# Kernel optimization log

Measured on AMD Instinct MI355X. Metric: run time of the kernel, lower is better.

Reference implementation:

```python
import jax, jax.numpy as jnp
import numpy as np

N_HEAD = 8
HEAD_DIM = 64
DIM = 512
INNER = N_HEAD * HEAD_DIM
ATT_THRESHOLD = 1e-4
SCALE = HEAD_DIM ** -0.5


def setup_inputs() -> dict:
    key = jax.random.key(0)
    ks = jax.random.split(key, 7)
    b, n, dn = 2, 2048, 2048
    fr = jax.random.normal(ks[0], (b, n, DIM), dtype=jnp.float32)
    dt = jax.random.normal(ks[1], (b, dn, DIM), dtype=jnp.float32)
    s = DIM ** -0.5
    Wq = jax.random.normal(ks[2], (DIM, INNER), dtype=jnp.float32) * s
    Wk = jax.random.normal(ks[3], (DIM, INNER), dtype=jnp.float32) * s
    Wv = jax.random.normal(ks[4], (DIM, INNER), dtype=jnp.float32) * s
    Wo = jax.random.normal(ks[5], (INNER, DIM), dtype=jnp.float32) * (INNER ** -0.5)
    bo = jax.random.normal(ks[6], (DIM,), dtype=jnp.float32) * 0.01
    return {"fr": fr, "dt": dt, "Wq": Wq, "Wk": Wk, "Wv": Wv, "Wo": Wo, "bo": bo}


def reference(fr, dt, Wq, Wk, Wv, Wo, bo):
    b, n, _ = fr.shape
    dn = dt.shape[1]
    # projections -> [b, seq, n_head, head_dim]
    q = (fr @ Wq).reshape(b, n, N_HEAD, HEAD_DIM)
    k = (dt @ Wk).reshape(b, dn, N_HEAD, HEAD_DIM)
    v = (dt @ Wv).reshape(b, dn, N_HEAD, HEAD_DIM)
    # full attention matrix [b, h, n, dn]
    scores = jnp.einsum('bihd,bjhd->bhij', q, k) * SCALE
    attn = jax.nn.softmax(scores, axis=-1)
    # torch .clip(t) with one positional arg clamps the MIN: max(attn, t)
    attn = jnp.maximum(attn, ATT_THRESHOLD) - ATT_THRESHOLD
    attn = attn / jnp.sum(attn, axis=-1, keepdims=True)
    out = jnp.einsum('bhij,bjhd->bihd', attn, v).reshape(b, n, INNER)
    return out @ Wo + bo
```

## Files before the change

### kernel.cpp

```cpp
#include <hip/hip_runtime.h>
#include <hip/hip_bf16.h>

#define BB 2
#define SEQ 2048
#define NHEAD 8
#define HD 64
#define ATT_T 1e-4f
#define QSCALE 0.18033688011112042f

typedef short s16x8 __attribute__((ext_vector_type(8)));
typedef float f32x16 __attribute__((ext_vector_type(16)));

#define MFMA32(a, b, c) __builtin_amdgcn_mfma_f32_32x32x16_bf16((a), (b), (c), 0, 0, 0)
#define EXP2(x) __builtin_amdgcn_exp2f(x)

__device__ __forceinline__ unsigned short bfr(float x) {
  __hip_bfloat16 h = __float2bfloat16(x);
  return __builtin_bit_cast(unsigned short, h);
}
__device__ __forceinline__ unsigned int packbf(float a, float b) {
  return (unsigned int)bfr(a) | ((unsigned int)bfr(b) << 16);
}
__device__ __forceinline__ void async16(const void* g, void* l) {
  __builtin_amdgcn_global_load_lds(
      (const __attribute__((address_space(1))) unsigned int*)g,
      (__attribute__((address_space(3))) unsigned int*)l, 16, 0, 0);
}

__global__ __launch_bounds__(256) void convT(const float* __restrict__ w0,
                                             const float* __restrict__ w1,
                                             const float* __restrict__ w2,
                                             const float* __restrict__ w3,
                                             unsigned short* __restrict__ o0,
                                             unsigned short* __restrict__ o1,
                                             unsigned short* __restrict__ o2,
                                             unsigned short* __restrict__ o3) {
  __shared__ float tle[64][65];
  const float* W = blockIdx.z == 0 ? w0 : blockIdx.z == 1 ? w1 : blockIdx.z == 2 ? w2 : w3;
  unsigned short* WT = blockIdx.z == 0 ? o0 : blockIdx.z == 1 ? o1 : blockIdx.z == 2 ? o2 : o3;
  const int r0 = blockIdx.y * 64, c0 = blockIdx.x * 64;
  const int tr = threadIdx.x >> 4;
  const int tc = threadIdx.x & 15;
  #pragma unroll
  for (int i = 0; i < 4; i++) {
    int r = tr + i * 16;
    float4 v = *(const float4*)(W + (size_t)(r0 + r) * 512 + c0 + tc * 4);
    tle[r][tc * 4 + 0] = v.x;
    tle[r][tc * 4 + 1] = v.y;
    tle[r][tc * 4 + 2] = v.z;
    tle[r][tc * 4 + 3] = v.w;
  }
  __syncthreads();
  #pragma unroll
  for (int i = 0; i < 4; i++) {
    int c = tr + i * 16;
    int rr = tc * 4;
    uint2 p;
    p.x = packbf(tle[rr + 0][c], tle[rr + 1][c]);
    p.y = packbf(tle[rr + 2][c], tle[rr + 3][c]);
    *(uint2*)(WT + (size_t)(c0 + c) * 512 + r0 + rr) = p;
  }
}

__global__ __launch_bounds__(256) void gemm_qkv(const float* __restrict__ frF,
                                                const float* __restrict__ dtF,
                                                const unsigned short* __restrict__ WqT,
                                                const unsigned short* __restrict__ WkT,
                                                const unsigned short* __restrict__ WvT,
                                                unsigned short* __restrict__ Qp,
                                                unsigned short* __restrict__ Kp,
                                                unsigned short* __restrict__ VTp) {
  __shared__ __align__(16) unsigned short smem[12288];
  unsigned short* Asm = smem;
  unsigned short* Bsm = smem + 4096;

  const int tid = threadIdx.x, lane = tid & 63, w = tid >> 6;
  const int l31 = lane & 31, lh = lane >> 5;
  const int m0 = blockIdx.y * 64, n0 = blockIdx.x * 128;
  const int z = blockIdx.z;
  const float* A = z == 0 ? frF : dtF;
  const unsigned short* BT = z == 0 ? WqT : (z == 1 ? WkT : WvT);
  unsigned short* OP = z == 0 ? Qp : (z == 1 ? Kp : VTp);
  const float scale = z == 0 ? QSCALE : 1.0f;

  const int arow = tid >> 2, arun = tid & 3;
  const float* Ap = A + (size_t)(m0 + arow) * 512 + arun * 8;
  const int aoff = (arow >> 5) * 1024 + (arun >> 1) * 512 + (arun & 1) * 256 + (arow & 31) * 8;

  auto stageB = [&](int kt, int buf) {
    const int k0 = kt * 32;
    #pragma unroll
    for (int i = 0; i < 2; i++) {
      int id = w * 2 + i;
      int g2 = id >> 1, ks = id & 1;
      async16(BT + (size_t)(n0 + g2 * 32 + l31) * 512 + k0 + ks * 16 + lh * 8,
              Bsm + buf * 4096 + g2 * 1024 + ks * 512);
    }
  };

  f32x16 acc[2];
  #pragma unroll
  for (int j = 0; j < 2; j++)
    #pragma unroll
    for (int r = 0; r < 16; r++) acc[j][r] = 0.f;

  float4 a0 = *(const float4*)(Ap + 0);
  float4 a1 = *(const float4*)(Ap + 4);
  stageB(0, 0);
  {
    uint4 w4;
    w4.x = packbf(a0.x, a0.y); w4.y = packbf(a0.z, a0.w);
    w4.z = packbf(a1.x, a1.y); w4.w = packbf(a1.z, a1.w);
    *(uint4*)(Asm + aoff) = w4;
  }
  a0 = *(const float4*)(Ap + 32);
  a1 = *(const float4*)(Ap + 36);

  for (int kt = 0; kt < 16; ++kt) {
    __syncthreads();
    if (kt + 1 < 16) {
      const int nb = (kt + 1) & 1;
      stageB(kt + 1, nb);
      uint4 w4;
      w4.x = packbf(a0.x, a0.y); w4.y = packbf(a0.z, a0.w);
      w4.z = packbf(a1.x, a1.y); w4.w = packbf(a1.z, a1.w);
      *(uint4*)(Asm + nb * 2048 + aoff) = w4;
      if (kt + 2 < 16) {
        a0 = *(const float4*)(Ap + (kt + 2) * 32);
        a1 = *(const float4*)(Ap + (kt + 2) * 32 + 4);
      }
    }
    const int buf = kt & 1;
    #pragma unroll
    for (int ks = 0; ks < 2; ++ks) {
      s16x8 af = *(const s16x8*)(Asm + buf * 2048 + (w & 1) * 1024 + ks * 512 + lane * 8);
      s16x8 b0 = *(const s16x8*)(Bsm + buf * 4096 + ((w >> 1) * 2 + 0) * 1024 + ks * 512 + lane * 8);
      s16x8 b1 = *(const s16x8*)(Bsm + buf * 4096 + ((w >> 1) * 2 + 1) * 1024 + ks * 512 + lane * 8);
      acc[0] = MFMA32(af, b0, acc[0]);
      acc[1] = MFMA32(af, b1, acc[1]);
    }
  }

  const int wm = (w & 1) * 32, wn = (w >> 1) * 64;
  const int bb = m0 >> 11, s0 = m0 & 2047;
  __syncthreads();
  if (z <= 1) {
    #pragma unroll
    for (int j = 0; j < 2; j++)
      #pragma unroll
      for (int r = 0; r < 16; r++) {
        int mm = wm + (r & 3) + 8 * (r >> 2) + 4 * lh;
        int nn = wn + j * 32 + l31;
        smem[mm * 136 + nn] = bfr(acc[j][r] * scale);
      }
    __syncthreads();
    #pragma unroll
    for (int it = 0; it < 4; ++it) {
      int c = tid + it * 256;
      int mm = c >> 4, seg = c & 15;
      uint4 vdat = *(const uint4*)(smem + mm * 136 + seg * 8);
      int n = n0 + seg * 8, h = n >> 6, d = n & 63;
      *(uint4*)(OP + ((size_t)((bb * NHEAD + h) * SEQ + s0 + mm)) * HD + d) = vdat;
    }
  } else {
    #pragma unroll
    for (int j = 0; j < 2; j++)
      #pragma unroll
      for (int r = 0; r < 16; r += 2) {
        int mm = wm + (r & 3) + 8 * (r >> 2) + 4 * lh;
        int nn = wn + j * 32 + l31;
        *(unsigned int*)(smem + nn * 72 + mm) = packbf(acc[j][r], acc[j][r + 1]);
      }
    __syncthreads();
    #pragma unroll
    for (int it = 0; it < 4; ++it) {
      int c = tid + it * 256;
      int nn = c >> 3, seg = c & 7;
      uint4 vdat = *(const uint4*)(smem + nn * 72 + seg * 8);
      int n = n0 + nn, h = n >> 6, d = n & 63;
      *(uint4*)(OP + ((size_t)((bb * NHEAD + h) * HD + d)) * SEQ + s0 + seg * 8) = vdat;
    }
  }
}

__device__ __forceinline__ void gemm_core64x128(const unsigned short* __restrict__ A,
                                                const unsigned short* __restrict__ BT,
                                                unsigned short* smem, int m0, int n0,
                                                int w, int lane, f32x16 (&acc)[2]) {
  unsigned short* Asm = smem;
  unsigned short* Bsm = smem + 4096;
  const int l31 = lane & 31, lh = lane >> 5;

  auto stage = [&](int kt, int buf) {
    const int k0 = kt * 32;
    #pragma unroll
    for (int i = 0; i < 3; i++) {
      int id = w * 3 + i;
      if (id < 4) {
        int g = id >> 1, ks = id & 1;
        async16(A + (size_t)(m0 + g * 32 + l31) * 512 + k0 + ks * 16 + lh * 8,
                Asm + buf * 2048 + g * 1024 + ks * 512);
      } else {
        int id2 = id - 4, g = id2 >> 1, ks = id2 & 1;
        async16(BT + (size_t)(n0 + g * 32 + l31) * 512 + k0 + ks * 16 + lh * 8,
                Bsm + buf * 4096 + g * 1024 + ks * 512);
      }
    }
  };

  stage(0, 0);
  for (int kt = 0; kt < 16; ++kt) {
    __syncthreads();
    if (kt + 1 < 16) stage(kt + 1, (kt + 1) & 1);
    const int buf = kt & 1;
    #pragma unroll
    for (int ks = 0; ks < 2; ++ks) {
      s16x8 af = *(const s16x8*)(Asm + buf * 2048 + (w & 1) * 1024 + ks * 512 + lane * 8);
      s16x8 b0 = *(const s16x8*)(Bsm + buf * 4096 + ((w >> 1) * 2 + 0) * 1024 + ks * 512 + lane * 8);
      s16x8 b1 = *(const s16x8*)(Bsm + buf * 4096 + ((w >> 1) * 2 + 1) * 1024 + ks * 512 + lane * 8);
      acc[0] = MFMA32(af, b0, acc[0]);
      acc[1] = MFMA32(af, b1, acc[1]);
    }
  }
}

__global__ __launch_bounds__(256) void gemm_out(const unsigned short* __restrict__ A,
                                                const unsigned short* __restrict__ BT,
                                                const float* __restrict__ bias,
                                                float* __restrict__ O) {
  __shared__ __align__(16) unsigned short smem[12288];
  const int tid = threadIdx.x, lane = tid & 63, w = tid >> 6;
  const int l31 = lane & 31, lh = lane >> 5;
  const int m0 = blockIdx.y * 64, n0 = blockIdx.x * 128;

  f32x16 acc[2];
  #pragma unroll
  for (int j = 0; j < 2; j++)
    #pragma unroll
    for (int r = 0; r < 16; r++) acc[j][r] = 0.f;

  gemm_core64x128(A, BT, smem, m0, n0, w, lane, acc);

  const int wm = (w & 1) * 32, wn = (w >> 1) * 64;
  #pragma unroll
  for (int j = 0; j < 2; j++) {
    float bv = bias[n0 + wn + j * 32 + l31];
    #pragma unroll
    for (int r = 0; r < 16; r++) {
      int mm = wm + (r & 3) + 8 * (r >> 2) + 4 * lh;
      O[(size_t)(m0 + mm) * 512 + n0 + wn + j * 32 + l31] = acc[j][r] + bv;
    }
  }
}

__global__ __launch_bounds__(512, 4) void attn_mfma(const unsigned short* __restrict__ Q,
                                                    const unsigned short* __restrict__ K,
                                                    const unsigned short* __restrict__ VT,
                                                    unsigned short* __restrict__ O) {
  __shared__ __align__(16) unsigned short kls[4][2][2048];
  __shared__ __align__(16) unsigned short vls[4][2][2048];
  __shared__ float larr[4][2][32];
  __shared__ float warr[4][2][32];

  const int tid = threadIdx.x;
  const int lane = tid & 63;
  const int w = tid >> 6;
  const int wq = w & 1, wk = w >> 1;
  const int l31 = lane & 31, lh = lane >> 5;

  const int qt = blockIdx.x & 31;
  const int bh = blockIdx.x >> 5;

  const unsigned short* Qh = Q + (size_t)bh * SEQ * HD;
  const unsigned short* Kh = K + (size_t)bh * SEQ * HD;
  const unsigned short* VTh = VT + (size_t)bh * HD * SEQ;

  const int qrow = qt * 64 + wq * 32 + l31;
  s16x8 qf[4];
  #pragma unroll
  for (int t = 0; t < 4; t++)
    qf[t] = *(const s16x8*)(Qh + (size_t)qrow * HD + 16 * t + 8 * lh);

  const int kbase = wk * 512;

  float l = 0.f;
  #pragma unroll
  for (int i = 0; i < 2; i++) {
    int tt = wq * 2 + i;
    async16(Kh + (size_t)(kbase + l31) * HD + tt * 16 + lh * 8, &kls[wk][0][tt * 512]);
  }
  for (int c = 0; c < 16; ++c) {
    __syncthreads();
    const int buf = c & 1;
    if (c + 1 < 16) {
      int key0 = kbase + (c + 1) * 32;
      #pragma unroll
      for (int i = 0; i < 2; i++) {
        int tt = wq * 2 + i;
        async16(Kh + (size_t)(key0 + l31) * HD + tt * 16 + lh * 8,
                &kls[wk][buf ^ 1][tt * 512]);
      }
    }
    f32x16 sc;
    #pragma unroll
    for (int r = 0; r < 16; r++) sc[r] = 0.f;
    #pragma unroll
    for (int tt = 0; tt < 4; tt++) {
      s16x8 kf = *(const s16x8*)&kls[wk][buf][tt * 512 + lane * 8];
      sc = MFMA32(kf, qf[tt], sc);
    }
    float s0 = 0.f, s1 = 0.f, s2 = 0.f, s3 = 0.f;
    #pragma unroll
    for (int r = 0; r < 4; r++) {
      s0 += EXP2(sc[r]);
      s1 += EXP2(sc[4 + r]);
      s2 += EXP2(sc[8 + r]);
      s3 += EXP2(sc[12 + r]);
    }
    l += (s0 + s1) + (s2 + s3);
  }
  l += __shfl_xor(l, 32);
  if (lh == 0) larr[wk][wq][l31] = l;

  f32x16 acc[2];
  #pragma unroll
  for (int j = 0; j < 2; j++)
    #pragma unroll
    for (int r = 0; r < 16; r++) acc[j][r] = 0.f;
  float wacc = 0.f;
  float tl = 0.f;

  #pragma unroll
  for (int i = 0; i < 2; i++) {
    int tt = wq * 2 + i;
    async16(Kh + (size_t)(kbase + l31) * HD + tt * 16 + lh * 8, &kls[wk][0][tt * 512]);
    async16(VTh + (size_t)(wq * 32 + l31) * SEQ + kbase + i * 16 + lh * 8,
            &vls[wk][0][(wq * 2 + i) * 512]);
  }
  for (int c = 0; c < 16; ++c) {
    __syncthreads();
    if (c == 0) {
      tl = ATT_T * (larr[0][wq][l31] + larr[1][wq][l31] +
                    larr[2][wq][l31] + larr[3][wq][l31]);
    }
    const int buf = c & 1;
    if (c + 1 < 16) {
      int key0 = kbase + (c + 1) * 32;
      #pragma unroll
      for (int i = 0; i < 2; i++) {
        int tt = wq * 2 + i;
        async16(Kh + (size_t)(key0 + l31) * HD + tt * 16 + lh * 8,
                &kls[wk][buf ^ 1][tt * 512]);
        async16(VTh + (size_t)(wq * 32 + l31) * SEQ + key0 + i * 16 + lh * 8,
                &vls[wk][buf ^ 1][(wq * 2 + i) * 512]);
      }
    }
    f32x16 sc;
    #pragma unroll
    for (int r = 0; r < 16; r++) sc[r] = 0.f;
    #pragma unroll
    for (int tt = 0; tt < 4; tt++) {
      s16x8 kf = *(const s16x8*)&kls[wk][buf][tt * 512 + lane * 8];
      sc = MFMA32(kf, qf[tt], sc);
    }
    uint2 quads[4];
    #pragma unroll
    for (int g = 0; g < 4; g++) {
      float u0 = fmaxf(EXP2(sc[4 * g + 0]) - tl, 0.f);
      float u1 = fmaxf(EXP2(sc[4 * g + 1]) - tl, 0.f);
      float u2 = fmaxf(EXP2(sc[4 * g + 2]) - tl, 0.f);
      float u3 = fmaxf(EXP2(sc[4 * g + 3]) - tl, 0.f);
      wacc += (u0 + u1) + (u2 + u3);
      quads[g].x = packbf(u0, u1);
      quads[g].y = packbf(u2, u3);
    }
    s16x8 pf[2];
    #pragma unroll
    for (int tp = 0; tp < 2; tp++) {
      uint2 ea, eb;
      ea.x = (unsigned)__shfl_xor((int)quads[2 * tp].x, 32);
      ea.y = (unsigned)__shfl_xor((int)quads[2 * tp].y, 32);
      eb.x = (unsigned)__shfl_xor((int)quads[2 * tp + 1].x, 32);
      eb.y = (unsigned)__shfl_xor((int)quads[2 * tp + 1].y, 32);
      uint4 fr;
      if (lh == 0) { fr.x = quads[2 * tp].x; fr.y = quads[2 * tp].y; fr.z = ea.x; fr.w = ea.y; }
      else         { fr.x = eb.x; fr.y = eb.y; fr.z = quads[2 * tp + 1].x; fr.w = quads[2 * tp + 1].y; }
      pf[tp] = __builtin_bit_cast(s16x8, fr);
    }
    #pragma unroll
    for (int kc = 0; kc < 2; kc++) {
      s16x8 v0 = *(const s16x8*)&vls[wk][buf][(0 * 2 + kc) * 512 + lane * 8];
      s16x8 v1 = *(const s16x8*)&vls[wk][buf][(1 * 2 + kc) * 512 + lane * 8];
      acc[0] = MFMA32(pf[kc], v0, acc[0]);
      acc[1] = MFMA32(pf[kc], v1, acc[1]);
    }
  }

  __syncthreads();
  wacc += __shfl_xor(wacc, 32);
  if (lh == 0) warr[wk][wq][l31] = wacc;

  float* plane = (float*)&kls[0][0][0];
  unsigned short* otile = &vls[0][0][0];

  if (wk >= 2) {
    const int p = wq * 2 + (wk - 2);
    #pragma unroll
    for (int j = 0; j < 2; j++)
      #pragma unroll
      for (int r = 0; r < 16; r++) {
        int ql = (r & 3) + 8 * (r >> 2) + 4 * lh;
        plane[p * 2048 + ql * 64 + j * 32 + l31] = acc[j][r];
      }
  }
  __syncthreads();
  if (wk < 2) {
    const int p = wq * 2 + wk;
    #pragma unroll
    for (int j = 0; j < 2; j++)
      #pragma unroll
      for (int r = 0; r < 16; r++) {
        int ql = (r & 3) + 8 * (r >> 2) + 4 * lh;
        acc[j][r] += plane[p * 2048 + ql * 64 + j * 32 + l31];
      }
  }
  __syncthreads();
  if (wk == 1) {
    #pragma unroll
    for (int j = 0; j < 2; j++)
      #pragma unroll
      for (int r = 0; r < 16; r++) {
        int ql = (r & 3) + 8 * (r >> 2) + 4 * lh;
        plane[wq * 2048 + ql * 64 + j * 32 + l31] = acc[j][r];
      }
  }
  __syncthreads();
  if (wk == 0) {
    #pragma unroll
    for (int j = 0; j < 2; j++)
      #pragma unroll
      for (int r = 0; r < 16; r++) {
        int ql = (r & 3) + 8 * (r >> 2) + 4 * lh;
        float wt = warr[0][wq][ql] + warr[1][wq][ql] + warr[2][wq][ql] + warr[3][wq][ql];
        float v = (acc[j][r] + plane[wq * 2048 + ql * 64 + j * 32 + l31]) / wt;
        otile[(wq * 32 + ql) * 64 + j * 32 + l31] = bfr(v);
      }
  }
  __syncthreads();
  const int b = bh >> 3, h = bh & 7;
  {
    int mm = tid >> 3, seg = tid & 7;
    uint4 vdat = *(const uint4*)(otile + mm * 64 + seg * 8);
    *(uint4*)(O + ((size_t)(b * SEQ + qt * 64 + mm)) * 512 + h * HD + seg * 8) = vdat;
  }
}

extern "C" void kernel_launch(void* const* d_in, const int* in_sizes, int n_in,
                              void* d_out, int out_size, void* d_ws, size_t ws_size,
                              hipStream_t stream) {
  const float* fr = (const float*)d_in[0];
  const float* dt = (const float*)d_in[1];
  const float* Wq = (const float*)d_in[2];
  const float* Wk = (const float*)d_in[3];
  const float* Wv = (const float*)d_in[4];
  const float* Wo = (const float*)d_in[5];
  const float* bo = (const float*)d_in[6];
  float* out = (float*)d_out;

  const size_t planeE = (size_t)BB * SEQ * 512;
  const size_t wE = 512 * 512;
  unsigned short* p = (unsigned short*)d_ws;
  unsigned short* WqT = p; p += wE;
  unsigned short* WkT = p; p += wE;
  unsigned short* WvT = p; p += wE;
  unsigned short* WoT = p; p += wE;
  unsigned short* Qp  = p; p += planeE;
  unsigned short* Kp  = p; p += planeE;
  unsigned short* VTp = p; p += planeE;
  unsigned short* aoB = p; p += planeE;

  convT<<<dim3(8, 8, 4), 256, 0, stream>>>(Wq, Wk, Wv, Wo, WqT, WkT, WvT, WoT);

  gemm_qkv<<<dim3(4, 64, 3), 256, 0, stream>>>(fr, dt, WqT, WkT, WvT, Qp, Kp, VTp);

  attn_mfma<<<BB * NHEAD * 32, 512, 0, stream>>>(Qp, Kp, VTp, aoB);

  gemm_out<<<dim3(4, 64), 256, 0, stream>>>(aoB, WoT, bo, out);
}
```

Baseline: 170.5 us.

## Replace LDS-staged async loads with direct global-to-register MFMA operand loads

The GEMM kernels and the attention kernel now load MFMA operand fragments straight from global memory into registers instead of double-buffering through LDS with global_load_lds and per-iteration barriers. This removes the __syncthreads in the main loops and cuts LDS use, which may raise occupancy. The attention grid is also remapped so blocks sharing a head are interleaved, and the launch-bounds occupancy hint is dropped. The trade-off is more redundant global/L2 traffic, because waves sharing K/V tiles each fetch them separately, and less latency hiding without explicit prefetch.

```diff
diff --git a/kernel.cpp b/kernel.cpp
--- a/kernel.cpp
+++ b/kernel.cpp
@@ -20,11 +20,6 @@
 }
 __device__ __forceinline__ unsigned int packbf(float a, float b) {
   return (unsigned int)bfr(a) | ((unsigned int)bfr(b) << 16);
-}
-__device__ __forceinline__ void async16(const void* g, void* l) {
-  __builtin_amdgcn_global_load_lds(
-      (const __attribute__((address_space(1))) unsigned int*)g,
-      (__attribute__((address_space(3))) unsigned int*)l, 16, 0, 0);
 }
 
 __global__ __launch_bounds__(256) void convT(const float* __restrict__ w0,
@@ -62,6 +57,31 @@
   }
 }
 
+__device__ __forceinline__ void gemm_loop_direct(const float* __restrict__ A,
+                                                 const unsigned short* __restrict__ BT,
+                                                 int m0, int n0, int w, int lane,
+                                                 f32x16 (&acc)[2]) {
+  const int l31 = lane & 31, lh = lane >> 5;
+  const int wm = (w & 1) * 32, wn = (w >> 1) * 64;
+  const float* Ar = A + (size_t)(m0 + wm + l31) * 512 + lh * 8;
+  const unsigned short* B0 = BT + (size_t)(n0 + wn + l31) * 512 + lh * 8;
+  const unsigned short* B1 = BT + (size_t)(n0 + wn + 32 + l31) * 512 + lh * 8;
+
+  #pragma unroll 4
+  for (int kt = 0; kt < 32; ++kt) {
+    float4 a0 = *(const float4*)(Ar + kt * 16);
+    float4 a1 = *(const float4*)(Ar + kt * 16 + 4);
+    s16x8 b0 = *(const s16x8*)(B0 + kt * 16);
+    s16x8 b1 = *(const s16x8*)(B1 + kt * 16);
+    uint4 af4;
+    af4.x = packbf(a0.x, a0.y); af4.y = packbf(a0.z, a0.w);
+    af4.z = packbf(a1.x, a1.y); af4.w = packbf(a1.z, a1.w);
+    s16x8 af = __builtin_bit_cast(s16x8, af4);
+    acc[0] = MFMA32(af, b0, acc[0]);
+    acc[1] = MFMA32(af, b1, acc[1]);
+  }
+}
+
 __global__ __launch_bounds__(256) void gemm_qkv(const float* __restrict__ frF,
                                                 const float* __restrict__ dtF,
                                                 const unsigned short* __restrict__ WqT,
@@ -70,10 +90,7 @@
                                                 unsigned short* __restrict__ Qp,
                                                 unsigned short* __restrict__ Kp,
                                                 unsigned short* __restrict__ VTp) {
-  __shared__ __align__(16) unsigned short smem[12288];
-  unsigned short* Asm = smem;
-  unsigned short* Bsm = smem + 4096;
-
+  __shared__ __align__(16) unsigned short smem[9216];
   const int tid = threadIdx.x, lane = tid & 63, w = tid >> 6;
   const int l31 = lane & 31, lh = lane >> 5;
   const int m0 = blockIdx.y * 64, n0 = blockIdx.x * 128;
@@ -83,67 +100,16 @@
   unsigned short* OP = z == 0 ? Qp : (z == 1 ? Kp : VTp);
   const float scale = z == 0 ? QSCALE : 1.0f;
 
-  const int arow = tid >> 2, arun = tid & 3;
-  const float* Ap = A + (size_t)(m0 + arow) * 512 + arun * 8;
-  const int aoff = (arow >> 5) * 1024 + (arun >> 1) * 512 + (arun & 1) * 256 + (arow & 31) * 8;
-
-  auto stageB = [&](int kt, int buf) {
-    const int k0 = kt * 32;
-    #pragma unroll
-    for (int i = 0; i < 2; i++) {
-      int id = w * 2 + i;
-      int g2 = id >> 1, ks = id & 1;
-      async16(BT + (size_t)(n0 + g2 * 32 + l31) * 512 + k0 + ks * 16 + lh * 8,
-              Bsm + buf * 4096 + g2 * 1024 + ks * 512);
-    }
-  };
-
   f32x16 acc[2];
   #pragma unroll
   for (int j = 0; j < 2; j++)
     #pragma unroll
     for (int r = 0; r < 16; r++) acc[j][r] = 0.f;
 
-  float4 a0 = *(const float4*)(Ap + 0);
-  float4 a1 = *(const float4*)(Ap + 4);
-  stageB(0, 0);
-  {
-    uint4 w4;
-    w4.x = packbf(a0.x, a0.y); w4.y = packbf(a0.z, a0.w);
-    w4.z = packbf(a1.x, a1.y); w4.w = packbf(a1.z, a1.w);
-    *(uint4*)(Asm + aoff) = w4;
-  }
-  a0 = *(const float4*)(Ap + 32);
-  a1 = *(const float4*)(Ap + 36);
-
-  for (int kt = 0; kt < 16; ++kt) {
-    __syncthreads();
-    if (kt + 1 < 16) {
-      const int nb = (kt + 1) & 1;
-      stageB(kt + 1, nb);
-      uint4 w4;
-      w4.x = packbf(a0.x, a0.y); w4.y = packbf(a0.z, a0.w);
-      w4.z = packbf(a1.x, a1.y); w4.w = packbf(a1.z, a1.w);
-      *(uint4*)(Asm + nb * 2048 + aoff) = w4;
-      if (kt + 2 < 16) {
-        a0 = *(const float4*)(Ap + (kt + 2) * 32);
-        a1 = *(const float4*)(Ap + (kt + 2) * 32 + 4);
-      }
-    }
-    const int buf = kt & 1;
-    #pragma unroll
-    for (int ks = 0; ks < 2; ++ks) {
-      s16x8 af = *(const s16x8*)(Asm + buf * 2048 + (w & 1) * 1024 + ks * 512 + lane * 8);
-      s16x8 b0 = *(const s16x8*)(Bsm + buf * 4096 + ((w >> 1) * 2 + 0) * 1024 + ks * 512 + lane * 8);
-      s16x8 b1 = *(const s16x8*)(Bsm + buf * 4096 + ((w >> 1) * 2 + 1) * 1024 + ks * 512 + lane * 8);
-      acc[0] = MFMA32(af, b0, acc[0]);
-      acc[1] = MFMA32(af, b1, acc[1]);
-    }
-  }
+  gemm_loop_direct(A, BT, m0, n0, w, lane, acc);
 
   const int wm = (w & 1) * 32, wn = (w >> 1) * 64;
   const int bb = m0 >> 11, s0 = m0 & 2047;
-  __syncthreads();
   if (z <= 1) {
     #pragma unroll
     for (int j = 0; j < 2; j++)
@@ -183,55 +149,18 @@
   }
 }
 
-__device__ __forceinline__ void gemm_core64x128(const unsigned short* __restrict__ A,
-                                                const unsigned short* __restrict__ BT,
-                                                unsigned short* smem, int m0, int n0,
-                                                int w, int lane, f32x16 (&acc)[2]) {
-  unsigned short* Asm = smem;
-  unsigned short* Bsm = smem + 4096;
-  const int l31 = lane & 31, lh = lane >> 5;
-
-  auto stage = [&](int kt, int buf) {
-    const int k0 = kt * 32;
-    #pragma unroll
-    for (int i = 0; i < 3; i++) {
-      int id = w * 3 + i;
-      if (id < 4) {
-        int g = id >> 1, ks = id & 1;
-        async16(A + (size_t)(m0 + g * 32 + l31) * 512 + k0 + ks * 16 + lh * 8,
-                Asm + buf * 2048 + g * 1024 + ks * 512);
-      } else {
-        int id2 = id - 4, g = id2 >> 1, ks = id2 & 1;
-        async16(BT + (size_t)(n0 + g * 32 + l31) * 512 + k0 + ks * 16 + lh * 8,
-                Bsm + buf * 4096 + g * 1024 + ks * 512);
-      }
-    }
-  };
-
-  stage(0, 0);
-  for (int kt = 0; kt < 16; ++kt) {
-    __syncthreads();
-    if (kt + 1 < 16) stage(kt + 1, (kt + 1) & 1);
-    const int buf = kt & 1;
-    #pragma unroll
-    for (int ks = 0; ks < 2; ++ks) {
-      s16x8 af = *(const s16x8*)(Asm + buf * 2048 + (w & 1) * 1024 + ks * 512 + lane * 8);
-      s16x8 b0 = *(const s16x8*)(Bsm + buf * 4096 + ((w >> 1) * 2 + 0) * 1024 + ks * 512 + lane * 8);
-      s16x8 b1 = *(const s16x8*)(Bsm + buf * 4096 + ((w >> 1) * 2 + 1) * 1024 + ks * 512 + lane * 8);
-      acc[0] = MFMA32(af, b0, acc[0]);
-      acc[1] = MFMA32(af, b1, acc[1]);
-    }
-  }
-}
-
 __global__ __launch_bounds__(256) void gemm_out(const unsigned short* __restrict__ A,
                                                 const unsigned short* __restrict__ BT,
                                                 const float* __restrict__ bias,
                                                 float* __restrict__ O) {
-  __shared__ __align__(16) unsigned short smem[12288];
   const int tid = threadIdx.x, lane = tid & 63, w = tid >> 6;
   const int l31 = lane & 31, lh = lane >> 5;
   const int m0 = blockIdx.y * 64, n0 = blockIdx.x * 128;
+  const int wm = (w & 1) * 32, wn = (w >> 1) * 64;
+
+  const unsigned short* Ar = A + (size_t)(m0 + wm + l31) * 512 + lh * 8;
+  const unsigned short* B0 = BT + (size_t)(n0 + wn + l31) * 512 + lh * 8;
+  const unsigned short* B1 = BT + (size_t)(n0 + wn + 32 + l31) * 512 + lh * 8;
 
   f32x16 acc[2];
   #pragma unroll
@@ -239,9 +168,15 @@
     #pragma unroll
     for (int r = 0; r < 16; r++) acc[j][r] = 0.f;
 
-  gemm_core64x128(A, BT, smem, m0, n0, w, lane, acc);
-
-  const int wm = (w & 1) * 32, wn = (w >> 1) * 64;
+  #pragma unroll 4
+  for (int kt = 0; kt < 32; ++kt) {
+    s16x8 af = *(const s16x8*)(Ar + kt * 16);
+    s16x8 b0 = *(const s16x8*)(B0 + kt * 16);
+    s16x8 b1 = *(const s16x8*)(B1 + kt * 16);
+    acc[0] = MFMA32(af, b0, acc[0]);
+    acc[1] = MFMA32(af, b1, acc[1]);
+  }
+
   #pragma unroll
   for (int j = 0; j < 2; j++) {
     float bv = bias[n0 + wn + j * 32 + l31];
@@ -253,12 +188,11 @@
   }
 }
 
-__global__ __launch_bounds__(512, 4) void attn_mfma(const unsigned short* __restrict__ Q,
-                                                    const unsigned short* __restrict__ K,
-                                                    const unsigned short* __restrict__ VT,
-                                                    unsigned short* __restrict__ O) {
-  __shared__ __align__(16) unsigned short kls[4][2][2048];
-  __shared__ __align__(16) unsigned short vls[4][2][2048];
+__global__ __launch_bounds__(512) void attn_mfma(const unsigned short* __restrict__ Q,
+                                                 const unsigned short* __restrict__ K,
+                                                 const unsigned short* __restrict__ VT,
+                                                 unsigned short* __restrict__ O) {
+  __shared__ float plane[4][2048];
   __shared__ float larr[4][2][32];
   __shared__ float warr[4][2][32];
 
@@ -268,8 +202,10 @@
   const int wq = w & 1, wk = w >> 1;
   const int l31 = lane & 31, lh = lane >> 5;
 
-  const int qt = blockIdx.x & 31;
-  const int bh = blockIdx.x >> 5;
+  const int bid = blockIdx.x;
+  const int g = bid & 7, j = bid >> 3;
+  const int bh = g * 2 + (j >> 5);
+  const int qt = j & 31;
 
   const unsigned short* Qh = Q + (size_t)bh * SEQ * HD;
   const unsigned short* Kh = K + (size_t)bh * SEQ * HD;
@@ -282,33 +218,23 @@
     qf[t] = *(const s16x8*)(Qh + (size_t)qrow * HD + 16 * t + 8 * lh);
 
   const int kbase = wk * 512;
+  const unsigned short* Kr = Kh + (size_t)(kbase + l31) * HD + lh * 8;
 
   float l = 0.f;
-  #pragma unroll
-  for (int i = 0; i < 2; i++) {
-    int tt = wq * 2 + i;
-    async16(Kh + (size_t)(kbase + l31) * HD + tt * 16 + lh * 8, &kls[wk][0][tt * 512]);
-  }
+  #pragma unroll 2
   for (int c = 0; c < 16; ++c) {
-    __syncthreads();
-    const int buf = c & 1;
-    if (c + 1 < 16) {
-      int key0 = kbase + (c + 1) * 32;
-      #pragma unroll
-      for (int i = 0; i < 2; i++) {
-        int tt = wq * 2 + i;
-        async16(Kh + (size_t)(key0 + l31) * HD + tt * 16 + lh * 8,
-                &kls[wk][buf ^ 1][tt * 512]);
-      }
-    }
+    const unsigned short* kp = Kr + (size_t)c * 32 * HD;
+    s16x8 k0 = *(const s16x8*)(kp + 0);
+    s16x8 k1 = *(const s16x8*)(kp + 16);
+    s16x8 k2 = *(const s16x8*)(kp + 32);
+    s16x8 k3 = *(const s16x8*)(kp + 48);
     f32x16 sc;
     #pragma unroll
     for (int r = 0; r < 16; r++) sc[r] = 0.f;
-    #pragma unroll
-    for (int tt = 0; tt < 4; tt++) {
-      s16x8 kf = *(const s16x8*)&kls[wk][buf][tt * 512 + lane * 8];
-      sc = MFMA32(kf, qf[tt], sc);
-    }
+    sc = MFMA32(k0, qf[0], sc);
+    sc = MFMA32(k1, qf[1], sc);
+    sc = MFMA32(k2, qf[2], sc);
+    sc = MFMA32(k3, qf[3], sc);
     float s0 = 0.f, s1 = 0.f, s2 = 0.f, s3 = 0.f;
     #pragma unroll
     for (int r = 0; r < 4; r++) {
@@ -321,58 +247,50 @@
   }
   l += __shfl_xor(l, 32);
   if (lh == 0) larr[wk][wq][l31] = l;
+  __syncthreads();
+
+  const float tl = ATT_T * (larr[0][wq][l31] + larr[1][wq][l31] +
+                            larr[2][wq][l31] + larr[3][wq][l31]);
 
   f32x16 acc[2];
   #pragma unroll
-  for (int j = 0; j < 2; j++)
-    #pragma unroll
-    for (int r = 0; r < 16; r++) acc[j][r] = 0.f;
+  for (int jj = 0; jj < 2; jj++)
+    #pragma unroll
+    for (int r = 0; r < 16; r++) acc[jj][r] = 0.f;
   float wacc = 0.f;
-  float tl = 0.f;
-
-  #pragma unroll
-  for (int i = 0; i < 2; i++) {
-    int tt = wq * 2 + i;
-    async16(Kh + (size_t)(kbase + l31) * HD + tt * 16 + lh * 8, &kls[wk][0][tt * 512]);
-    async16(VTh + (size_t)(wq * 32 + l31) * SEQ + kbase + i * 16 + lh * 8,
-            &vls[wk][0][(wq * 2 + i) * 512]);
-  }
+
+  const unsigned short* V0 = VTh + (size_t)(l31) * SEQ + kbase + lh * 8;
+  const unsigned short* V1 = VTh + (size_t)(32 + l31) * SEQ + kbase + lh * 8;
+
+  #pragma unroll 2
   for (int c = 0; c < 16; ++c) {
-    __syncthreads();
-    if (c == 0) {
-      tl = ATT_T * (larr[0][wq][l31] + larr[1][wq][l31] +
-                    larr[2][wq][l31] + larr[3][wq][l31]);
-    }
-    const int buf = c & 1;
-    if (c + 1 < 16) {
-      int key0 = kbase + (c + 1) * 32;
-      #pragma unroll
-      for (int i = 0; i < 2; i++) {
-        int tt = wq * 2 + i;
-        async16(Kh + (size_t)(key0 + l31) * HD + tt * 16 + lh * 8,
-                &kls[wk][buf ^ 1][tt * 512]);
-        async16(VTh + (size_t)(wq * 32 + l31) * SEQ + key0 + i * 16 + lh * 8,
-                &vls[wk][buf ^ 1][(wq * 2 + i) * 512]);
-      }
-    }
+    const unsigned short* kp = Kr + (size_t)c * 32 * HD;
+    s16x8 k0 = *(const s16x8*)(kp + 0);
+    s16x8 k1 = *(const s16x8*)(kp + 16);
+    s16x8 k2 = *(const s16x8*)(kp + 32);
+    s16x8 k3 = *(const s16x8*)(kp + 48);
+    s16x8 va0 = *(const s16x8*)(V0 + c * 32);
+    s16x8 va1 = *(const s16x8*)(V0 + c * 32 + 16);
+    s16x8 vb0 = *(const s16x8*)(V1 + c * 32);
+    s16x8 vb1 = *(const s16x8*)(V1 + c * 32 + 16);
     f32x16 sc;
     #pragma unroll
     for (int r = 0; r < 16; r++) sc[r] = 0.f;
-    #pragma unroll
-    for (int tt = 0; tt < 4; tt++) {
-      s16x8 kf = *(const s16x8*)&kls[wk][buf][tt * 512 + lane * 8];
-      sc = MFMA32(kf, qf[tt], sc);
-    }
+    sc = MFMA32(k0, qf[0], sc);
+    sc = MFMA32(k1, qf[1], sc);
+    sc = MFMA32(k2, qf[2], sc);
+    sc = MFMA32(k3, qf[3], sc);
+
     uint2 quads[4];
     #pragma unroll
-    for (int g = 0; g < 4; g++) {
-      float u0 = fmaxf(EXP2(sc[4 * g + 0]) - tl, 0.f);
-      float u1 = fmaxf(EXP2(sc[4 * g + 1]) - tl, 0.f);
-      float u2 = fmaxf(EXP2(sc[4 * g + 2]) - tl, 0.f);
-      float u3 = fmaxf(EXP2(sc[4 * g + 3]) - tl, 0.f);
+    for (int gq = 0; gq < 4; gq++) {
+      float u0 = fmaxf(EXP2(sc[4 * gq + 0]) - tl, 0.f);
+      float u1 = fmaxf(EXP2(sc[4 * gq + 1]) - tl, 0.f);
+      float u2 = fmaxf(EXP2(sc[4 * gq + 2]) - tl, 0.f);
+      float u3 = fmaxf(EXP2(sc[4 * gq + 3]) - tl, 0.f);
       wacc += (u0 + u1) + (u2 + u3);
-      quads[g].x = packbf(u0, u1);
-      quads[g].y = packbf(u2, u3);
+      quads[gq].x = packbf(u0, u1);
+      quads[gq].y = packbf(u2, u3);
     }
     s16x8 pf[2];
     #pragma unroll
@@ -387,63 +305,57 @@
       else         { fr.x = eb.x; fr.y = eb.y; fr.z = quads[2 * tp + 1].x; fr.w = quads[2 * tp + 1].y; }
       pf[tp] = __builtin_bit_cast(s16x8, fr);
     }
-    #pragma unroll
-    for (int kc = 0; kc < 2; kc++) {
-      s16x8 v0 = *(const s16x8*)&vls[wk][buf][(0 * 2 + kc) * 512 + lane * 8];
-      s16x8 v1 = *(const s16x8*)&vls[wk][buf][(1 * 2 + kc) * 512 + lane * 8];
-      acc[0] = MFMA32(pf[kc], v0, acc[0]);
-      acc[1] = MFMA32(pf[kc], v1, acc[1]);
-    }
-  }
-
-  __syncthreads();
+    acc[0] = MFMA32(pf[0], va0, acc[0]);
+    acc[0] = MFMA32(pf[1], va1, acc[0]);
+    acc[1] = MFMA32(pf[0], vb0, acc[1]);
+    acc[1] = MFMA32(pf[1], vb1, acc[1]);
+  }
+
   wacc += __shfl_xor(wacc, 32);
   if (lh == 0) warr[wk][wq][l31] = wacc;
 
-  float* plane = (float*)&kls[0][0][0];
-  unsigned short* otile = &vls[0][0][0];
-
   if (wk >= 2) {
     const int p = wq * 2 + (wk - 2);
     #pragma unroll
-    for (int j = 0; j < 2; j++)
+    for (int jj = 0; jj < 2; jj++)
       #pragma unroll
       for (int r = 0; r < 16; r++) {
         int ql = (r & 3) + 8 * (r >> 2) + 4 * lh;
-        plane[p * 2048 + ql * 64 + j * 32 + l31] = acc[j][r];
+        plane[p][ql * 64 + jj * 32 + l31] = acc[jj][r];
       }
   }
   __syncthreads();
   if (wk < 2) {
     const int p = wq * 2 + wk;
     #pragma unroll
-    for (int j = 0; j < 2; j++)
+    for (int jj = 0; jj < 2; jj++)
       #pragma unroll
       for (int r = 0; r < 16; r++) {
         int ql = (r & 3) + 8 * (r >> 2) + 4 * lh;
-        acc[j][r] += plane[p * 2048 + ql * 64 + j * 32 + l31];
+        acc[jj][r] += plane[p][ql * 64 + jj * 32 + l31];
       }
   }
   __syncthreads();
   if (wk == 1) {
     #pragma unroll
-    for (int j = 0; j < 2; j++)
+    for (int jj = 0; jj < 2; jj++)
       #pragma unroll
       for (int r = 0; r < 16; r++) {
         int ql = (r & 3) + 8 * (r >> 2) + 4 * lh;
-        plane[wq * 2048 + ql * 64 + j * 32 + l31] = acc[j][r];
-      }
-  }
-  __syncthreads();
+        plane[wq][ql * 64 + jj * 32 + l31] = acc[jj][r];
+      }
+  }
+  __syncthreads();
+  unsigned short* otile = (unsigned short*)&plane[2][0];
   if (wk == 0) {
     #pragma unroll
-    for (int j = 0; j < 2; j++)
+    for (int jj = 0; jj < 2; jj++)
       #pragma unroll
       for (int r = 0; r < 16; r++) {
         int ql = (r & 3) + 8 * (r >> 2) + 4 * lh;
         float wt = warr[0][wq][ql] + warr[1][wq][ql] + warr[2][wq][ql] + warr[3][wq][ql];
-        float v = (acc[j][r] + plane[wq * 2048 + ql * 64 + j * 32 + l31]) / wt;
-        otile[(wq * 32 + ql) * 64 + j * 32 + l31] = bfr(v);
+        float v = (acc[jj][r] + plane[wq][ql * 64 + jj * 32 + l31]) / wt;
+        otile[(wq * 32 + ql) * 64 + jj * 32 + l31] = bfr(v);
       }
   }
   __syncthreads();
```

New measurement: 238.3 us. 39.7% more time.

## Pre-convert activations to bf16, use BK=64 async GEMM core, remap attention blocks

Applied to the files above, without the earlier changes.

Adds a kernel that converts fr and dt to bf16 up front, so the QKV GEMM can stage both A and B with async global-to-LDS loads. QKV and output projections now share one GEMM core with K-tile 64, which halves the k-loop iterations and barriers at the cost of doubled LDS. The attention grid is remapped so consecutive blocks span different heads, with loop variables renamed. This adds an extra launch and a bf16 round trip of the activations through memory.

```diff
diff --git a/kernel.cpp b/kernel.cpp
--- a/kernel.cpp
+++ b/kernel.cpp
@@ -25,6 +25,20 @@
   __builtin_amdgcn_global_load_lds(
       (const __attribute__((address_space(1))) unsigned int*)g,
       (__attribute__((address_space(3))) unsigned int*)l, 16, 0, 0);
+}
+
+__global__ __launch_bounds__(256) void conv_bf16(const float* __restrict__ x0,
+                                                 const float* __restrict__ x1,
+                                                 unsigned short* __restrict__ y0,
+                                                 unsigned short* __restrict__ y1) {
+  const float* x = blockIdx.y ? x1 : x0;
+  unsigned short* y = blockIdx.y ? y1 : y0;
+  size_t i = ((size_t)blockIdx.x * 256 + threadIdx.x) * 4;
+  float4 v = *(const float4*)(x + i);
+  uint2 p;
+  p.x = packbf(v.x, v.y);
+  p.y = packbf(v.z, v.w);
+  *(uint2*)(y + i) = p;
 }
 
 __global__ __launch_bounds__(256) void convT(const float* __restrict__ w0,
@@ -62,84 +76,73 @@
   }
 }
 
-__global__ __launch_bounds__(256) void gemm_qkv(const float* __restrict__ frF,
-                                                const float* __restrict__ dtF,
+__device__ __forceinline__ void gemm_core_bk64(const unsigned short* __restrict__ A,
+                                               const unsigned short* __restrict__ BT,
+                                               unsigned short* smem, int m0, int n0,
+                                               int w, int lane, f32x16 (&acc)[2]) {
+  unsigned short* Asm = smem;
+  unsigned short* Bsm = smem + 8192;
+  const int l31 = lane & 31, lh = lane >> 5;
+
+  auto stage = [&](int kt, int buf) {
+    const int k0 = kt * 64;
+    #pragma unroll
+    for (int i = 0; i < 2; i++) {
+      int r = w * 2 + i, g = r >> 2, ks = r & 3;
+      async16(A + (size_t)(m0 + g * 32 + l31) * 512 + k0 + ks * 16 + lh * 8,
+              Asm + buf * 4096 + r * 512);
+    }
+    #pragma unroll
+    for (int i = 0; i < 4; i++) {
+      int r = w * 4 + i, gn = r >> 2, ks = r & 3;
+      async16(BT + (size_t)(n0 + gn * 32 + l31) * 512 + k0 + ks * 16 + lh * 8,
+              Bsm + buf * 8192 + r * 512);
+    }
+  };
+
+  stage(0, 0);
+  for (int kt = 0; kt < 8; ++kt) {
+    __syncthreads();
+    if (kt + 1 < 8) stage(kt + 1, (kt + 1) & 1);
+    const int buf = kt & 1;
+    const unsigned short* as = Asm + buf * 4096 + (w & 1) * 2048;
+    const unsigned short* bs = Bsm + buf * 8192 + (w >> 1) * 4096;
+    #pragma unroll
+    for (int ks = 0; ks < 4; ++ks) {
+      s16x8 af = *(const s16x8*)(as + ks * 512 + lane * 8);
+      s16x8 b0 = *(const s16x8*)(bs + ks * 512 + lane * 8);
+      s16x8 b1 = *(const s16x8*)(bs + 2048 + ks * 512 + lane * 8);
+      acc[0] = MFMA32(af, b0, acc[0]);
+      acc[1] = MFMA32(af, b1, acc[1]);
+    }
+  }
+}
+
+__global__ __launch_bounds__(256) void gemm_qkv(const unsigned short* __restrict__ frB,
+                                                const unsigned short* __restrict__ dtB,
                                                 const unsigned short* __restrict__ WqT,
                                                 const unsigned short* __restrict__ WkT,
                                                 const unsigned short* __restrict__ WvT,
                                                 unsigned short* __restrict__ Qp,
                                                 unsigned short* __restrict__ Kp,
                                                 unsigned short* __restrict__ VTp) {
-  __shared__ __align__(16) unsigned short smem[12288];
-  unsigned short* Asm = smem;
-  unsigned short* Bsm = smem + 4096;
-
+  __shared__ __align__(16) unsigned short smem[24576];
   const int tid = threadIdx.x, lane = tid & 63, w = tid >> 6;
   const int l31 = lane & 31, lh = lane >> 5;
   const int m0 = blockIdx.y * 64, n0 = blockIdx.x * 128;
   const int z = blockIdx.z;
-  const float* A = z == 0 ? frF : dtF;
+  const unsigned short* A = z == 0 ? frB : dtB;
   const unsigned short* BT = z == 0 ? WqT : (z == 1 ? WkT : WvT);
   unsigned short* OP = z == 0 ? Qp : (z == 1 ? Kp : VTp);
   const float scale = z == 0 ? QSCALE : 1.0f;
 
-  const int arow = tid >> 2, arun = tid & 3;
-  const float* Ap = A + (size_t)(m0 + arow) * 512 + arun * 8;
-  const int aoff = (arow >> 5) * 1024 + (arun >> 1) * 512 + (arun & 1) * 256 + (arow & 31) * 8;
-
-  auto stageB = [&](int kt, int buf) {
-    const int k0 = kt * 32;
-    #pragma unroll
-    for (int i = 0; i < 2; i++) {
-      int id = w * 2 + i;
-      int g2 = id >> 1, ks = id & 1;
-      async16(BT + (size_t)(n0 + g2 * 32 + l31) * 512 + k0 + ks * 16 + lh * 8,
-              Bsm + buf * 4096 + g2 * 1024 + ks * 512);
-    }
-  };
-
   f32x16 acc[2];
   #pragma unroll
   for (int j = 0; j < 2; j++)
     #pragma unroll
     for (int r = 0; r < 16; r++) acc[j][r] = 0.f;
 
-  float4 a0 = *(const float4*)(Ap + 0);
-  float4 a1 = *(const float4*)(Ap + 4);
-  stageB(0, 0);
-  {
-    uint4 w4;
-    w4.x = packbf(a0.x, a0.y); w4.y = packbf(a0.z, a0.w);
-    w4.z = packbf(a1.x, a1.y); w4.w = packbf(a1.z, a1.w);
-    *(uint4*)(Asm + aoff) = w4;
-  }
-  a0 = *(const float4*)(Ap + 32);
-  a1 = *(const float4*)(Ap + 36);
-
-  for (int kt = 0; kt < 16; ++kt) {
-    __syncthreads();
-    if (kt + 1 < 16) {
-      const int nb = (kt + 1) & 1;
-      stageB(kt + 1, nb);
-      uint4 w4;
-      w4.x = packbf(a0.x, a0.y); w4.y = packbf(a0.z, a0.w);
-      w4.z = packbf(a1.x, a1.y); w4.w = packbf(a1.z, a1.w);
-      *(uint4*)(Asm + nb * 2048 + aoff) = w4;
-      if (kt + 2 < 16) {
-        a0 = *(const float4*)(Ap + (kt + 2) * 32);
-        a1 = *(const float4*)(Ap + (kt + 2) * 32 + 4);
-      }
-    }
-    const int buf = kt & 1;
-    #pragma unroll
-    for (int ks = 0; ks < 2; ++ks) {
-      s16x8 af = *(const s16x8*)(Asm + buf * 2048 + (w & 1) * 1024 + ks * 512 + lane * 8);
-      s16x8 b0 = *(const s16x8*)(Bsm + buf * 4096 + ((w >> 1) * 2 + 0) * 1024 + ks * 512 + lane * 8);
-      s16x8 b1 = *(const s16x8*)(Bsm + buf * 4096 + ((w >> 1) * 2 + 1) * 1024 + ks * 512 + lane * 8);
-      acc[0] = MFMA32(af, b0, acc[0]);
-      acc[1] = MFMA32(af, b1, acc[1]);
-    }
-  }
+  gemm_core_bk64(A, BT, smem, m0, n0, w, lane, acc);
 
   const int wm = (w & 1) * 32, wn = (w >> 1) * 64;
   const int bb = m0 >> 11, s0 = m0 & 2047;
@@ -183,52 +186,11 @@
   }
 }
 
-__device__ __forceinline__ void gemm_core64x128(const unsigned short* __restrict__ A,
-                                                const unsigned short* __restrict__ BT,
-                                                unsigned short* smem, int m0, int n0,
-                                                int w, int lane, f32x16 (&acc)[2]) {
-  unsigned short* Asm = smem;
-  unsigned short* Bsm = smem + 4096;
-  const int l31 = lane & 31, lh = lane >> 5;
-
-  auto stage = [&](int kt, int buf) {
-    const int k0 = kt * 32;
-    #pragma unroll
-    for (int i = 0; i < 3; i++) {
-      int id = w * 3 + i;
-      if (id < 4) {
-        int g = id >> 1, ks = id & 1;
-        async16(A + (size_t)(m0 + g * 32 + l31) * 512 + k0 + ks * 16 + lh * 8,
-                Asm + buf * 2048 + g * 1024 + ks * 512);
-      } else {
-        int id2 = id - 4, g = id2 >> 1, ks = id2 & 1;
-        async16(BT + (size_t)(n0 + g * 32 + l31) * 512 + k0 + ks * 16 + lh * 8,
-                Bsm + buf * 4096 + g * 1024 + ks * 512);
-      }
-    }
-  };
-
-  stage(0, 0);
-  for (int kt = 0; kt < 16; ++kt) {
-    __syncthreads();
-    if (kt + 1 < 16) stage(kt + 1, (kt + 1) & 1);
-    const int buf = kt & 1;
-    #pragma unroll
-    for (int ks = 0; ks < 2; ++ks) {
-      s16x8 af = *(const s16x8*)(Asm + buf * 2048 + (w & 1) * 1024 + ks * 512 + lane * 8);
-      s16x8 b0 = *(const s16x8*)(Bsm + buf * 4096 + ((w >> 1) * 2 + 0) * 1024 + ks * 512 + lane * 8);
-      s16x8 b1 = *(const s16x8*)(Bsm + buf * 4096 + ((w >> 1) * 2 + 1) * 1024 + ks * 512 + lane * 8);
-      acc[0] = MFMA32(af, b0, acc[0]);
-      acc[1] = MFMA32(af, b1, acc[1]);
-    }
-  }
-}
-
 __global__ __launch_bounds__(256) void gemm_out(const unsigned short* __restrict__ A,
                                                 const unsigned short* __restrict__ BT,
                                                 const float* __restrict__ bias,
                                                 float* __restrict__ O) {
-  __shared__ __align__(16) unsigned short smem[12288];
+  __shared__ __align__(16) unsigned short smem[24576];
   const int tid = threadIdx.x, lane = tid & 63, w = tid >> 6;
   const int l31 = lane & 31, lh = lane >> 5;
   const int m0 = blockIdx.y * 64, n0 = blockIdx.x * 128;
@@ -239,7 +201,7 @@
     #pragma unroll
     for (int r = 0; r < 16; r++) acc[j][r] = 0.f;
 
-  gemm_core64x128(A, BT, smem, m0, n0, w, lane, acc);
+  gemm_core_bk64(A, BT, smem, m0, n0, w, lane, acc);
 
   const int wm = (w & 1) * 32, wn = (w >> 1) * 64;
   #pragma unroll
@@ -268,8 +230,10 @@
   const int wq = w & 1, wk = w >> 1;
   const int l31 = lane & 31, lh = lane >> 5;
 
-  const int qt = blockIdx.x & 31;
-  const int bh = blockIdx.x >> 5;
+  const int bid = blockIdx.x;
+  const int g = bid & 7, j = bid >> 3;
+  const int bh = g * 2 + (j >> 5);
+  const int qt = j & 31;
 
   const unsigned short* Qh = Q + (size_t)bh * SEQ * HD;
   const unsigned short* Kh = K + (size_t)bh * SEQ * HD;
@@ -324,9 +288,9 @@
 
   f32x16 acc[2];
   #pragma unroll
-  for (int j = 0; j < 2; j++)
-    #pragma unroll
-    for (int r = 0; r < 16; r++) acc[j][r] = 0.f;
+  for (int jj = 0; jj < 2; jj++)
+    #pragma unroll
+    for (int r = 0; r < 16; r++) acc[jj][r] = 0.f;
   float wacc = 0.f;
   float tl = 0.f;
 
@@ -365,14 +329,14 @@
     }
     uint2 quads[4];
     #pragma unroll
-    for (int g = 0; g < 4; g++) {
-      float u0 = fmaxf(EXP2(sc[4 * g + 0]) - tl, 0.f);
-      float u1 = fmaxf(EXP2(sc[4 * g + 1]) - tl, 0.f);
-      float u2 = fmaxf(EXP2(sc[4 * g + 2]) - tl, 0.f);
-      float u3 = fmaxf(EXP2(sc[4 * g + 3]) - tl, 0.f);
+    for (int gq = 0; gq < 4; gq++) {
+      float u0 = fmaxf(EXP2(sc[4 * gq + 0]) - tl, 0.f);
+      float u1 = fmaxf(EXP2(sc[4 * gq + 1]) - tl, 0.f);
+      float u2 = fmaxf(EXP2(sc[4 * gq + 2]) - tl, 0.f);
+      float u3 = fmaxf(EXP2(sc[4 * gq + 3]) - tl, 0.f);
       wacc += (u0 + u1) + (u2 + u3);
-      quads[g].x = packbf(u0, u1);
-      quads[g].y = packbf(u2, u3);
+      quads[gq].x = packbf(u0, u1);
+      quads[gq].y = packbf(u2, u3);
     }
     s16x8 pf[2];
     #pragma unroll
@@ -406,44 +370,44 @@
   if (wk >= 2) {
     const int p = wq * 2 + (wk - 2);
     #pragma unroll
-    for (int j = 0; j < 2; j++)
+    for (int jj = 0; jj < 2; jj++)
       #pragma unroll
       for (int r = 0; r < 16; r++) {
         int ql = (r & 3) + 8 * (r >> 2) + 4 * lh;
-        plane[p * 2048 + ql * 64 + j * 32 + l31] = acc[j][r];
+        plane[p * 2048 + ql * 64 + jj * 32 + l31] = acc[jj][r];
       }
   }
   __syncthreads();
   if (wk < 2) {
     const int p = wq * 2 + wk;
     #pragma unroll
-    for (int j = 0; j < 2; j++)
+    for (int jj = 0; jj < 2; jj++)
       #pragma unroll
       for (int r = 0; r < 16; r++) {
         int ql = (r & 3) + 8 * (r >> 2) + 4 * lh;
-        acc[j][r] += plane[p * 2048 + ql * 64 + j * 32 + l31];
+        acc[jj][r] += plane[p * 2048 + ql * 64 + jj * 32 + l31];
       }
   }
   __syncthreads();
   if (wk == 1) {
     #pragma unroll
-    for (int j = 0; j < 2; j++)
+    for (int jj = 0; jj < 2; jj++)
       #pragma unroll
       for (int r = 0; r < 16; r++) {
         int ql = (r & 3) + 8 * (r >> 2) + 4 * lh;
-        plane[wq * 2048 + ql * 64 + j * 32 + l31] = acc[j][r];
+        plane[wq * 2048 + ql * 64 + jj * 32 + l31] = acc[jj][r];
       }
   }
   __syncthreads();
   if (wk == 0) {
     #pragma unroll
-    for (int j = 0; j < 2; j++)
+    for (int jj = 0; jj < 2; jj++)
       #pragma unroll
       for (int r = 0; r < 16; r++) {
         int ql = (r & 3) + 8 * (r >> 2) + 4 * lh;
         float wt = warr[0][wq][ql] + warr[1][wq][ql] + warr[2][wq][ql] + warr[3][wq][ql];
-        float v = (acc[j][r] + plane[wq * 2048 + ql * 64 + j * 32 + l31]) / wt;
-        otile[(wq * 32 + ql) * 64 + j * 32 + l31] = bfr(v);
+        float v = (acc[jj][r] + plane[wq * 2048 + ql * 64 + jj * 32 + l31]) / wt;
+        otile[(wq * 32 + ql) * 64 + jj * 32 + l31] = bfr(v);
       }
   }
   __syncthreads();
@@ -470,6 +434,8 @@
   const size_t planeE = (size_t)BB * SEQ * 512;
   const size_t wE = 512 * 512;
   unsigned short* p = (unsigned short*)d_ws;
+  unsigned short* frB = p; p += planeE;
+  unsigned short* dtB = p; p += planeE;
   unsigned short* WqT = p; p += wE;
   unsigned short* WkT = p; p += wE;
   unsigned short* WvT = p; p += wE;
@@ -479,9 +445,10 @@
   unsigned short* VTp = p; p += planeE;
   unsigned short* aoB = p; p += planeE;
 
+  conv_bf16<<<dim3(2048, 2), 256, 0, stream>>>(fr, dt, frB, dtB);
   convT<<<dim3(8, 8, 4), 256, 0, stream>>>(Wq, Wk, Wv, Wo, WqT, WkT, WvT, WoT);
 
-  gemm_qkv<<<dim3(4, 64, 3), 256, 0, stream>>>(fr, dt, WqT, WkT, WvT, Qp, Kp, VTp);
+  gemm_qkv<<<dim3(4, 64, 3), 256, 0, stream>>>(frB, dtB, WqT, WkT, WvT, Qp, Kp, VTp);
 
   attn_mfma<<<BB * NHEAD * 32, 512, 0, stream>>>(Qp, Kp, VTp, aoB);
 
```

Result: no change. 172.5 us (+1.1%).
